# Optimization experiments

Measured on AMD Instinct MI355X. Metric: run time of the kernel, lower is better.

The kernel has to match this reference:

```python
import jax, jax.numpy as jnp
import numpy as np

N_WIRES = 12
N_LAYERS = 2
BATCH = 512


def _apply_1q(state, U, wire, n):
    """Apply a 2x2 gate U ([2,2] shared or [B,2,2] per-sample) on `wire`."""
    B = state.shape[0]
    pre, post = 2 ** wire, 2 ** (n - wire - 1)
    s = state.reshape(B, pre, 2, post)
    if U.ndim == 3:
        s = jnp.einsum('bij,bpjq->bpiq', U, s)
    else:
        s = jnp.einsum('ij,bpjq->bpiq', U, s)
    return s.reshape(B, 2 ** n)


def _apply_cnot(state, ctrl, tgt, n):
    B = state.shape[0]
    a, b = (ctrl, tgt) if ctrl < tgt else (tgt, ctrl)
    pre, mid, post = 2 ** a, 2 ** (b - a - 1), 2 ** (n - b - 1)
    s = state.reshape(B, pre, 2, mid, 2, post)
    if ctrl < tgt:
        # control at axis 2, target at axis 4: flip target where control==1
        s = jnp.stack([s[:, :, 0], s[:, :, 1, :, ::-1]], axis=2)
    else:
        # control at axis 4, target at axis 2
        s = jnp.stack([s[:, :, :, :, 0], s[:, :, ::-1, :, 1]], axis=4)
    return s.reshape(B, 2 ** n)


def _rot_matrices(var):
    """PennyLane Rot(phi,theta,omega)=RZ(omega)RY(theta)RZ(phi); var [L,n,3] -> [L,n,2,2]."""
    phi, theta, omega = var[..., 0], var[..., 1], var[..., 2]
    c = jnp.cos(theta / 2).astype(jnp.complex64)
    si = jnp.sin(theta / 2).astype(jnp.complex64)
    ep = jnp.exp(-0.5j * (phi + omega).astype(jnp.complex64))   # e^{-i(phi+omega)/2}
    em = jnp.exp(-0.5j * (phi - omega).astype(jnp.complex64))   # e^{-i(phi-omega)/2}
    U00 = ep * c
    U01 = -jnp.conj(em) * si
    U10 = em * si
    U11 = jnp.conj(ep) * c
    return jnp.stack([jnp.stack([U00, U01], -1), jnp.stack([U10, U11], -1)], -2)


def _circuit(x, var, n, L):
    """Batched statevector sim: RY encoding + StronglyEntanglingLayers + PauliZ expvals."""
    B = x.shape[0]
    state = jnp.zeros((B, 2 ** n), jnp.complex64).at[:, 0].set(1.0)
    # per-sample RY encoding
    c = jnp.cos(x / 2).astype(jnp.complex64)
    s = jnp.sin(x / 2).astype(jnp.complex64)
    for w in range(n):
        Ry = jnp.stack([jnp.stack([c[:, w], -s[:, w]], -1),
                        jnp.stack([s[:, w], c[:, w]], -1)], -2)  # [B,2,2]
        state = _apply_1q(state, Ry, w, n)
    rots = _rot_matrices(var)
    for l in range(L):
        for w in range(n):
            state = _apply_1q(state, rots[l, w], w, n)
        r = (l % (n - 1)) + 1 if n > 1 else 0  # default StronglyEntanglingLayers ranges
        if r:
            for w in range(n):
                state = _apply_cnot(state, w, (w + r) % n, n)
    probs = jnp.real(state * jnp.conj(state)).astype(jnp.float32)  # [B, 2^n]
    idx = jnp.arange(2 ** n)
    bits = (idx[None, :] >> (n - 1 - jnp.arange(n))[:, None]) & 1   # wire w -> bit n-1-w
    zsign = (1.0 - 2.0 * bits).astype(jnp.float32)                  # [n, 2^n]
    return probs @ zsign.T  # [B, n] PauliZ expvals


def setup_inputs() -> dict:
    key = jax.random.key(0)
    k1, k2, k3, k4 = jax.random.split(key, 4)
    x = jax.random.normal(k1, (BATCH, N_WIRES), dtype=jnp.float32)
    var_params = jax.random.normal(k2, (N_LAYERS, N_WIRES, 3), dtype=jnp.float32)
    head_w = jax.random.normal(k3, (1, N_WIRES), dtype=jnp.float32) / np.sqrt(N_WIRES)
    head_b = jax.random.normal(k4, (1,), dtype=jnp.float32) / np.sqrt(N_WIRES)
    return {"x": x, "var_params": var_params, "head_w": head_w, "head_b": head_b}


def reference(x, var_params, head_w, head_b):
    q = _circuit(x, var_params, N_WIRES, N_LAYERS)  # [B, num_wires]
    return (q @ head_w.T + head_b)[:, 0]            # [B]
```

## Files before the change

### kernel.cpp

```cpp
#include <hip/hip_runtime.h>

constexpr int NSTR = 2664;

struct TabT { unsigned ty[NSTR]; unsigned me[NSTR]; };
struct SlT  { int len[12]; int list[12][6]; };

constexpr SlT build_s() {
    SlT s{};
    for (int wp = 0; wp < 12; ++wp) {
        unsigned z = 1u << wp;
        for (int w = 11; w >= 0; --w) {
            int c = w, tg = (w + 2) % 12;
            if ((z >> tg) & 1u) z ^= 1u << c;
        }
        int ns = 0;
        for (int k = 0; k < 12; ++k) if ((z >> k) & 1u) s.list[wp][ns++] = k;
        s.len[wp] = ns;
        for (int i = ns; i < 6; ++i) s.list[wp][i] = 12;
    }
    return s;
}

constexpr TabT build_tab() {
    TabT t{};
    SlT s = build_s();
    int idx = 0;
    for (int wp = 0; wp < 12; ++wp) {
        int ns = s.len[wp];
        int total = 1;
        for (int i = 0; i < ns; ++i) total *= 3;
        for (int n = 0; n < total; ++n) {
            unsigned xm = 0, zm = 0, choices = 0; int sg = 0, nn = n;
            for (int i = 0; i < ns; ++i) {
                int d = nn % 3; nn /= 3;
                choices |= (unsigned)d << (2 * i);
                int k = s.list[wp][i];
                if (d == 0 || d == 1) xm |= 1u << k;
                if (d == 1 || d == 2) zm |= 1u << k;
            }
            for (int w = 11; w >= 0; --w) {
                int a = w, b2 = (w + 1) % 12;
                unsigned xa = (xm >> a) & 1u, zb = (zm >> b2) & 1u;
                unsigned xb = (xm >> b2) & 1u, za = (zm >> a) & 1u;
                sg ^= (int)(xa & zb & (xb ^ za ^ 1u));
                xm ^= xa << b2;
                zm ^= zb << a;
            }
            unsigned ty = 0;
            for (int k = 0; k < 12; ++k) {
                unsigned xx = (xm >> k) & 1u, zz = (zm >> k) & 1u;
                unsigned tp = (xx & zz) ? 2u : (xx ? 1u : (zz ? 3u : 0u));
                ty |= tp << (2 * k);
            }
            t.ty[idx] = ty;
            t.me[idx] = (unsigned)wp | ((unsigned)sg << 4) | (choices << 5);
            ++idx;
        }
    }
    return t;
}

__constant__ TabT g_tab = build_tab();
__constant__ SlT  g_sl  = build_s();

__global__ __launch_bounds__(512)
void qnn_kernel(const float* __restrict__ x, const float* __restrict__ var,
                const float* __restrict__ hw, const float* __restrict__ hb,
                float* __restrict__ out)
{
    __shared__ float mq[12][4];
    __shared__ float qq[13][4];
    __shared__ float hh[12];
    __shared__ float wavesum[8];

    const int t = threadIdx.x, b = blockIdx.x;
    const int lane = t & 63, wid = t >> 6;

    if (wid == 0 && lane < 12) {
        const int w = lane;
        const float phi = var[w*3+0], theta = var[w*3+1], omega = var[w*3+2];
        float st, ct; sincosf(0.5f*theta, &st, &ct);
        float sp, cp; sincosf(-0.5f*(phi+omega), &sp, &cp);
        float sm, cm; sincosf(-0.5f*(phi-omega), &sm, &cm);
        float s_, c_; sincosf(0.5f * x[b*12 + w], &s_, &c_);
        const float v0r = cp*ct*c_ - cm*st*s_;
        const float v0i = sp*ct*c_ + sm*st*s_;
        const float v1r = cm*st*c_ + cp*ct*s_;
        const float v1i = sm*st*c_ - sp*ct*s_;
        mq[w][0] = 1.0f;
        mq[w][1] = 2.0f*(v0r*v1r + v0i*v1i);
        mq[w][2] = 2.0f*(v0r*v1i - v0i*v1r);
        mq[w][3] = (v0r*v0r + v0i*v0i) - (v1r*v1r + v1i*v1i);
        hh[w] = hw[w];
    } else if (wid == 1 && lane < 13) {
        if (lane < 12) {
            const int w = lane, g = 12 + w;
            const float phi = var[g*3+0], theta = var[g*3+1], omega = var[g*3+2];
            float st, ct; sincosf(0.5f*theta, &st, &ct);
            float sp, cp; sincosf(-0.5f*(phi+omega), &sp, &cp);
            float sm, cm; sincosf(-0.5f*(phi-omega), &sm, &cm);
            const float u00r =  cp*ct, u00i =  sp*ct;
            const float u01r = -cm*st, u01i =  sm*st;
            const float u10r =  cm*st, u10i =  sm*st;
            const float u11r =  cp*ct, u11i = -sp*ct;
            const float B01r = (u00r*u01r + u00i*u01i) - (u10r*u11r + u10i*u11i);
            const float B01i = (u00r*u01i - u00i*u01r) - (u10r*u11i - u10i*u11r);
            qq[w][0] = 1.0f;
            qq[w][1] = B01r;
            qq[w][2] = -B01i;
            qq[w][3] = (u00r*u00r + u00i*u00i) - (u10r*u10r + u10i*u10i);
        } else {
            qq[12][0] = qq[12][1] = qq[12][2] = qq[12][3] = 1.0f;
        }
    }
    __syncthreads();

    float acc = 0.0f;
    for (int i = t; i < NSTR; i += 512) {
        const unsigned ty = g_tab.ty[i];
        const unsigned me = g_tab.me[i];
        const int wp = me & 15;
        const unsigned ch = me >> 5;
        float cf = hh[wp];
        #pragma unroll
        for (int ii = 0; ii < 6; ++ii) {
            const int k = g_sl.list[wp][ii];
            const int d = (ch >> (2*ii)) & 3;
            cf *= qq[k][d + 1];
        }
        if ((me >> 4) & 1) cf = -cf;
        #pragma unroll
        for (int k = 0; k < 12; ++k)
            cf *= mq[k][(ty >> (2*k)) & 3];
        acc += cf;
    }

    #pragma unroll
    for (int off = 32; off > 0; off >>= 1) acc += __shfl_down(acc, off, 64);
    if (lane == 0) wavesum[wid] = acc;
    __syncthreads();
    if (t == 0) {
        float r = hb[0];
        #pragma unroll
        for (int wv = 0; wv < 8; ++wv) r += wavesum[wv];
        out[b] = r;
    }
}

extern "C" void kernel_launch(void* const* d_in, const int* in_sizes, int n_in,
                              void* d_out, int out_size, void* d_ws, size_t ws_size,
                              hipStream_t stream) {
    const float* x   = (const float*)d_in[0];
    const float* var = (const float*)d_in[1];
    const float* hw  = (const float*)d_in[2];
    const float* hb  = (const float*)d_in[3];
    float* out = (float*)d_out;
    qnn_kernel<<<out_size, 512, 0, stream>>>(x, var, hw, hb, out);
}
```

Baseline: 9.986 us.

## Parallelize per-block sincos across threads and halve block size to 256

The 84 sincos evaluations per block are spread across 84 threads and stored in shared memory, replacing the serial chain of four sincos calls per lane in waves 0 and 1. The block size drops from 512 to 256 threads, so each thread processes about 11 table entries instead of about 6. The shorter serial setup should shrink the critical-path prologue, and smaller blocks may fit more blocks per CU across the 512-block grid. The cost is an extra __syncthreads and a longer per-thread loop.

```diff
diff --git a/kernel.cpp b/kernel.cpp
--- a/kernel.cpp
+++ b/kernel.cpp
@@ -1,6 +1,7 @@
 #include <hip/hip_runtime.h>
 
 constexpr int NSTR = 2664;
+constexpr int BT   = 256;
 
 struct TabT { unsigned ty[NSTR]; unsigned me[NSTR]; };
 struct SlT  { int len[12]; int list[12][6]; };
@@ -63,26 +64,43 @@
 __constant__ TabT g_tab = build_tab();
 __constant__ SlT  g_sl  = build_s();
 
-__global__ __launch_bounds__(512)
+__global__ __launch_bounds__(BT)
 void qnn_kernel(const float* __restrict__ x, const float* __restrict__ var,
                 const float* __restrict__ hw, const float* __restrict__ hb,
                 float* __restrict__ out)
 {
+    __shared__ float2 sc[84];
     __shared__ float mq[12][4];
     __shared__ float qq[13][4];
     __shared__ float hh[12];
-    __shared__ float wavesum[8];
+    __shared__ float wavesum[4];
 
     const int t = threadIdx.x, b = blockIdx.x;
     const int lane = t & 63, wid = t >> 6;
 
+    if (t < 84) {
+        const int w = t / 7, r = t - w * 7;
+        float ang;
+        if (r == 3) ang = 0.5f * x[b*12 + w];
+        else {
+            const int g = (r < 3) ? w : 12 + w;
+            const int rr = (r < 3) ? r : r - 4;
+            const float phi = var[g*3+0], theta = var[g*3+1], omega = var[g*3+2];
+            ang = (rr == 0) ? 0.5f * theta
+                : (rr == 1) ? -0.5f * (phi + omega)
+                            : -0.5f * (phi - omega);
+        }
+        float s_, c_; sincosf(ang, &s_, &c_);
+        sc[t] = make_float2(s_, c_);
+    }
+    __syncthreads();
+
     if (wid == 0 && lane < 12) {
         const int w = lane;
-        const float phi = var[w*3+0], theta = var[w*3+1], omega = var[w*3+2];
-        float st, ct; sincosf(0.5f*theta, &st, &ct);
-        float sp, cp; sincosf(-0.5f*(phi+omega), &sp, &cp);
-        float sm, cm; sincosf(-0.5f*(phi-omega), &sm, &cm);
-        float s_, c_; sincosf(0.5f * x[b*12 + w], &s_, &c_);
+        const float st = sc[w*7+0].x, ct = sc[w*7+0].y;
+        const float sp = sc[w*7+1].x, cp = sc[w*7+1].y;
+        const float sm = sc[w*7+2].x, cm = sc[w*7+2].y;
+        const float s_ = sc[w*7+3].x, c_ = sc[w*7+3].y;
         const float v0r = cp*ct*c_ - cm*st*s_;
         const float v0i = sp*ct*c_ + sm*st*s_;
         const float v1r = cm*st*c_ + cp*ct*s_;
@@ -94,11 +112,10 @@
         hh[w] = hw[w];
     } else if (wid == 1 && lane < 13) {
         if (lane < 12) {
-            const int w = lane, g = 12 + w;
-            const float phi = var[g*3+0], theta = var[g*3+1], omega = var[g*3+2];
-            float st, ct; sincosf(0.5f*theta, &st, &ct);
-            float sp, cp; sincosf(-0.5f*(phi+omega), &sp, &cp);
-            float sm, cm; sincosf(-0.5f*(phi-omega), &sm, &cm);
+            const int w = lane;
+            const float st = sc[w*7+4].x, ct = sc[w*7+4].y;
+            const float sp = sc[w*7+5].x, cp = sc[w*7+5].y;
+            const float sm = sc[w*7+6].x, cm = sc[w*7+6].y;
             const float u00r =  cp*ct, u00i =  sp*ct;
             const float u01r = -cm*st, u01i =  sm*st;
             const float u10r =  cm*st, u10i =  sm*st;
@@ -116,7 +133,7 @@
     __syncthreads();
 
     float acc = 0.0f;
-    for (int i = t; i < NSTR; i += 512) {
+    for (int i = t; i < NSTR; i += BT) {
         const unsigned ty = g_tab.ty[i];
         const unsigned me = g_tab.me[i];
         const int wp = me & 15;
@@ -139,12 +156,8 @@
     for (int off = 32; off > 0; off >>= 1) acc += __shfl_down(acc, off, 64);
     if (lane == 0) wavesum[wid] = acc;
     __syncthreads();
-    if (t == 0) {
-        float r = hb[0];
-        #pragma unroll
-        for (int wv = 0; wv < 8; ++wv) r += wavesum[wv];
-        out[b] = r;
-    }
+    if (t == 0)
+        out[b] = wavesum[0] + wavesum[1] + wavesum[2] + wavesum[3] + hb[0];
 }
 
 extern "C" void kernel_launch(void* const* d_in, const int* in_sizes, int n_in,
@@ -155,5 +168,5 @@
     const float* hw  = (const float*)d_in[2];
     const float* hb  = (const float*)d_in[3];
     float* out = (float*)d_out;
-    qnn_kernel<<<out_size, 512, 0, stream>>>(x, var, hw, hb, out);
+    qnn_kernel<<<out_size, BT, 0, stream>>>(x, var, hw, hb, out);
 }
```

Result: slower. 11.36 us (+13.8%).
